# Performance work log

Hardware: AMD Instinct MI355X
Metric: run time of the kernel (lower is better)

The kernel has to match this reference:

```python
import jax, jax.numpy as jnp
import numpy as np

B, Z, U, L, T, D_IN = 64, 512, 2048, 3, 32, 90  # batch, latent, lstm_units, layers, seq_len, output_depth


def setup_inputs() -> dict:
    key = jax.random.key(0)
    ks = jax.random.split(key, 2 + 3 * L + 2)
    s = 0.02
    inp = {"z": jax.random.normal(ks[0], (B, Z), dtype=jnp.float32)}
    inp["w_init"] = jax.random.normal(ks[1], (Z, U * L * 2), dtype=jnp.float32) * s
    inp["b_init"] = jnp.zeros((U * L * 2,), dtype=jnp.float32)
    for i in range(L):
        din = (D_IN + Z) if i == 0 else U
        inp[f"k{i}"] = jax.random.normal(ks[2 + 3 * i], (din, 4 * U), dtype=jnp.float32) * s
        inp[f"rk{i}"] = jax.random.normal(ks[3 + 3 * i], (U, 4 * U), dtype=jnp.float32) * s
        inp[f"b{i}"] = jnp.zeros((4 * U,), dtype=jnp.float32)
    inp["w_out"] = jax.random.normal(ks[-2], (U, D_IN), dtype=jnp.float32) * s
    inp["b_out"] = jnp.zeros((D_IN,), dtype=jnp.float32)
    return inp


def lstm_cell(x, h, c, k, rk, b):
    # Keras LSTMCell: gates in (i, f, g, o) order
    zg = x @ k + h @ rk + b
    i, f, g, o = jnp.split(zg, 4, axis=-1)
    c = jax.nn.sigmoid(f) * c + jax.nn.sigmoid(i) * jnp.tanh(g)
    h = jax.nn.sigmoid(o) * jnp.tanh(c)
    return h, c


def reference(z, w_init, b_init, k0, rk0, b0, k1, rk1, b1, k2, rk2, b2, w_out, b_out):
    Bsz = z.shape[0]
    # z -> initial (h, c) per layer: reshape [B, L, 2, U] -> [L, 2, B, U]
    st = (z @ w_init + b_init).reshape(Bsz, L, 2, U).transpose(1, 2, 0, 3)
    carry = tuple((st[i, 0], st[i, 1]) for i in range(L))
    # generation feeds dummy zero step_input concat z, constant across time
    x = jnp.concatenate([jnp.zeros((Bsz, D_IN), z.dtype), z], axis=-1)
    params = ((k0, rk0, b0), (k1, rk1, b1), (k2, rk2, b2))

    def step(carry, _):
        cin = x
        new = []
        for (k, rk, b), (h, c) in zip(params, carry):
            h, c = lstm_cell(cin, h, c, k, rk, b)
            new.append((h, c))
            cin = h
        logits = cin @ w_out + b_out  # [B, D_IN]
        return tuple(new), logits

    _, ys = jax.lax.scan(step, carry, None, length=T)  # [T, B, D_IN]
    return ys.transpose(1, 0, 2)  # [B, T, D_IN]
```

## Files before the change

### kernel.cpp

```cpp
#include <hip/hip_runtime.h>
#include <cstdint>

#define B_   64
#define Z_   512
#define U_   2048
#define T_   32
#define DIN_ 90
#define G4_  8192
#define STLD 12288

using bf16x8 = __attribute__((ext_vector_type(8))) short;
using f32x4  = __attribute__((ext_vector_type(4))) float;

#define MFMA(a, b, c) __builtin_amdgcn_mfma_f32_16x16x32_bf16((a), (b), (c), 0, 0, 0)

__device__ __forceinline__ unsigned short f2bf(float f) {
    unsigned int u = __float_as_uint(f);
    unsigned int r = (u + 0x7FFFu + ((u >> 16) & 1u)) >> 16;
    return (unsigned short)r;
}
__device__ __forceinline__ float sigf(float x) { return 1.f / (1.f + expf(-x)); }

__device__ __forceinline__ void gld16(const void* g, void* l) {
    __builtin_amdgcn_global_load_lds(
        (const __attribute__((address_space(1))) unsigned int*)g,
        (__attribute__((address_space(3))) unsigned int*)l, 16, 0, 0);
}

#define GEMM_PROLOG()                                                        \
    size_t ag0, ag1, wg0; unsigned al0, al1, wl0;                            \
    {                                                                        \
        int kb0 = (l & 15) << 4;                                             \
        int r0 = wv * 4 + (l >> 4);                        \
        int sw0 = kb0 ^ ((r0 & 7) << 4);                                     \
        ag0 = (size_t)r0 * U_ + (sw0 >> 1);                                  \
        al0 = wv * 1024;                                                     \
        int r1 = 32 + r0;                                 \
        int sw1 = kb0 ^ ((r1 & 7) << 4);                                     \
        ag1 = (size_t)r1 * U_ + (sw1 >> 1);                                  \
        al1 = 8192 + wv * 1024;                                              \
        int rw = r0;                                       \
        int sww = kb0 ^ ((rw & 7) << 4);                                     \
        wg0 = (size_t)(prow0 + rw) * U_ + (sww >> 1);                        \
        wl0 = 16384 + wv * 1024;                                             \
    }                                                                        \
    int aoff[4], woff[4];                                                    \
    {                                                                        \
        const int lkb = (l >> 4) << 4;                                       \
        _Pragma("unroll")                                                    \
        for (int ks = 0; ks < 4; ++ks) {                                     \
            int kb = ks * 64 + lkb;                                          \
            int ar = rq * 16 + lr, wr = ch * 16 + lr;                        \
            aoff[ks] = ar * 256 + (kb ^ ((ar & 7) << 4));                    \
            woff[ks] = 16384 + wr * 256 + (kb ^ ((wr & 7) << 4));            \
        }                                                                    \
    }

#define ISSUE(Ap, Wp, tt) do {                                               \
        const int k0_ = (tt) * 128;                                          \
        char* sb_ = stg + ((tt) % 3) * 24576;                                \
        gld16((Ap) + ag0 + k0_, sb_ + al0);                                  \
        gld16((Ap) + ag1 + k0_, sb_ + al1);                                  \
        gld16((Wp) + wg0 + k0_, sb_ + wl0);                                  \
    } while (0)

#define GEMM_LOOP(Ap, Wp)                                                    \
    ISSUE(Ap, Wp, 0);                                                        \
    ISSUE(Ap, Wp, 1);                                                        \
    for (int tt = 0; tt < 16; ++tt) {                                        \
        if (tt < 15) asm volatile("s_waitcnt vmcnt(3)" ::: "memory");        \
        else         asm volatile("s_waitcnt vmcnt(0)" ::: "memory");        \
        __builtin_amdgcn_s_barrier();                                        \
        if (tt + 2 < 16) ISSUE(Ap, Wp, tt + 2);                              \
        const char* sb = stg + (tt % 3) * 24576;                             \
        _Pragma("unroll")                                                    \
        for (int ks = 0; ks < 4; ++ks) {                                     \
            bf16x8 av = *(const bf16x8*)(sb + aoff[ks]);                     \
            bf16x8 wf = *(const bf16x8*)(sb + woff[ks]);                     \
            acc = MFMA(av, wf, acc);                                         \
        }                                                                    \
    }

#define EPI_ZG(ZG) do {                                                      \
        const int l4_ = (l >> 4) << 2;                                       \
        _Pragma("unroll")                                                    \
        for (int r = 0; r < 4; ++r) {                                        \
            int row = rq * 16 + l4_ + r;                                     \
            int col = prow0 + ch * 16 + lr;                                  \
            __builtin_nontemporal_store(acc[r], &(ZG)[(size_t)row * G4_ + col]); \
        }                                                                    \
    } while (0)

#define EPI_FILL_PLAIN() do {                                                \
        __syncthreads();                         \
        const int l4_ = (l >> 4) << 2;                                       \
        _Pragma("unroll")                                                    \
        for (int r = 0; r < 4; ++r)                                          \
            sg[rq * 16 + l4_ + r][ch * 16 + lr] = acc[r];                    \
    } while (0)

#define EPI_FILL_ZG(ZGIN) do {                                               \
        __syncthreads();                         \
        const int l4_ = (l >> 4) << 2;                                       \
        _Pragma("unroll")                                                    \
        for (int r = 0; r < 4; ++r) {                                        \
            int row = rq * 16 + l4_ + r;                                     \
            int col = prow0 + ch * 16 + lr;                                  \
            sg[row][ch * 16 + lr] =                                          \
                acc[r] + __builtin_nontemporal_load(&(ZGIN)[(size_t)row * G4_ + col]); \
        }                                                                    \
    } while (0)

#define EPI_GATE(BASEEXPR, CST, HNEW) do {                                   \
        __syncthreads();                                                     \
        const int b = t >> 3, uu = t & 7;                                    \
        const int u = blockIdx.x * 8 + uu;                                   \
        float g[4];                                                          \
        _Pragma("unroll")                                                    \
        for (int gi = 0; gi < 4; ++gi)                                       \
            g[gi] = sg[b][gi * 8 + uu] + (BASEEXPR);                         \
        float* cp = (CST) + (size_t)b * U_ + u;                              \
        const float c_ = *cp;                                                \
        const float cn = sigf(g[1]) * c_ + sigf(g[0]) * tanhf(g[2]);         \
        const float hn = sigf(g[3]) * tanhf(cn);                             \
        *cp = cn;                                                            \
        (HNEW)[(size_t)b * U_ + u] = f2bf(hn);                               \
    } while (0)

#define STEP_COMMON()                                                        \
    __shared__ char stg[3 * 24576];                                          \
    auto sg = reinterpret_cast<float(*)[33]>(stg + 2 * 24576);               \
    const int t = threadIdx.x, wv = t >> 6, l = t & 63;                      \
    const int prow0 = blockIdx.x * 32;                                       \
    const int rq = wv & 3, ch = wv >> 2, lr = l & 15;


__global__ __launch_bounds__(256) void transpose_cvt(const float* __restrict__ W,
                                                     unsigned short* __restrict__ Wt,
                                                     int K, int N, int row_off)
{
    __shared__ float tile[32][33];
    const int nb = blockIdx.x * 32, kb = blockIdx.y * 32;
    const int tx = threadIdx.x & 31, ty = threadIdx.x >> 5;
    #pragma unroll
    for (int i = 0; i < 4; ++i)
        tile[ty + i * 8][tx] = W[(size_t)(row_off + kb + ty + i * 8) * N + nb + tx];
    __syncthreads();
    #pragma unroll
    for (int i = 0; i < 4; ++i)
        Wt[(size_t)(nb + ty + i * 8) * K + kb + tx] = f2bf(tile[tx][ty + i * 8]);
}

__global__ __launch_bounds__(256) void transpose_cvt_packed(const float* __restrict__ W,
                                                            unsigned short* __restrict__ Wt)
{
    __shared__ float tile[32][33];
    const int nb = blockIdx.x * 32, kb = blockIdx.y * 32;
    const int tx = threadIdx.x & 31, ty = threadIdx.x >> 5;
    #pragma unroll
    for (int i = 0; i < 4; ++i)
        tile[ty + i * 8][tx] = W[(size_t)(kb + ty + i * 8) * G4_ + nb + tx];
    __syncthreads();
    #pragma unroll
    for (int i = 0; i < 4; ++i) {
        int n = nb + ty + i * 8;
        int g = n >> 11, u = n & 2047;
        int prow = ((u >> 3) << 5) + (g << 3) + (u & 7);
        Wt[(size_t)prow * U_ + kb + tx] = f2bf(tile[tx][ty + i * 8]);
    }
}

__global__ __launch_bounds__(256) void wout_cvt(const float* __restrict__ w_out,
                                                unsigned short* __restrict__ w_outT)
{
    int i = blockIdx.x * 256 + threadIdx.x;
    int d = i >> 11, k = i & 2047;
    w_outT[i] = (d < DIN_) ? f2bf(w_out[(size_t)k * DIN_ + d]) : (unsigned short)0;
}

__global__ __launch_bounds__(256) void cvt_z(const float* __restrict__ z,
                                             unsigned short* __restrict__ zb)
{
    int i = blockIdx.x * 256 + threadIdx.x;
    zb[i] = f2bf(z[i]);
}

__global__ __launch_bounds__(256) void hcinit(const float* __restrict__ st,
                                              unsigned short* __restrict__ h0,
                                              unsigned short* __restrict__ h1,
                                              unsigned short* __restrict__ h2s0,
                                              float* __restrict__ c0,
                                              float* __restrict__ c1,
                                              float* __restrict__ c2)
{
    int idx = blockIdx.x * 256 + threadIdx.x;
    int u = idx & 2047, b = (idx >> 11) & 63, ly = idx >> 17;
    float hv = st[(size_t)b * STLD + ly * 4096 + u];
    float cv = st[(size_t)b * STLD + ly * 4096 + 2048 + u];
    unsigned short* h = (ly == 0) ? h0 : (ly == 1) ? h1 : h2s0;
    float* c = (ly == 0) ? c0 : (ly == 1) ? c1 : c2;
    h[(size_t)b * 2048 + u] = f2bf(hv);
    c[(size_t)b * 2048 + u] = cv;
}

__global__ __launch_bounds__(256) void gemm_plain(const unsigned short* __restrict__ A, int K,
                                                  const unsigned short* __restrict__ Wt,
                                                  const float* __restrict__ bias,
                                                  float* __restrict__ out, int ldo)
{
    const int t = threadIdx.x, wv = t >> 6, l = t & 63;
    const int wm = (wv >> 1) * 32, n0 = blockIdx.x * 64 + (wv & 1) * 32;
    const int lr = l & 15, lk = (l >> 4) * 8;
    f32x4 acc[2][2] = {};
    for (int kt = 0; kt < K; kt += 32) {
        bf16x8 a0 = *(const bf16x8*)(A + (size_t)(wm + lr) * K + kt + lk);
        bf16x8 a1 = *(const bf16x8*)(A + (size_t)(wm + 16 + lr) * K + kt + lk);
        bf16x8 w0 = *(const bf16x8*)(Wt + (size_t)(n0 + lr) * K + kt + lk);
        bf16x8 w1 = *(const bf16x8*)(Wt + (size_t)(n0 + 16 + lr) * K + kt + lk);
        acc[0][0] = MFMA(a0, w0, acc[0][0]);
        acc[0][1] = MFMA(a0, w1, acc[0][1]);
        acc[1][0] = MFMA(a1, w0, acc[1][0]);
        acc[1][1] = MFMA(a1, w1, acc[1][1]);
    }
    #pragma unroll
    for (int mi = 0; mi < 2; ++mi)
        #pragma unroll
        for (int ni = 0; ni < 2; ++ni)
            #pragma unroll
            for (int r = 0; r < 4; ++r) {
                int row = wm + mi * 16 + (l >> 4) * 4 + r;
                int col = n0 + ni * 16 + lr;
                out[(size_t)row * ldo + col] = acc[mi][ni][r] + bias[col];
            }
}

__global__ __launch_bounds__(512) void stepX0(
    const unsigned short* __restrict__ h0old, const unsigned short* __restrict__ rk0P,
    const float* __restrict__ xk0, float* __restrict__ cst0,
    unsigned short* __restrict__ h0new,
    const unsigned short* __restrict__ h1old, const unsigned short* __restrict__ rk1P,
    float* __restrict__ zg1)
{
    STEP_COMMON();
    const int z = blockIdx.y;
    const unsigned short* A = (z == 0) ? h0old : h1old;
    const unsigned short* W = (z == 0) ? rk0P : rk1P;

    GEMM_PROLOG();
    f32x4 acc = {};
    GEMM_LOOP(A, W);

    if (z == 0) {
        EPI_FILL_PLAIN();
        EPI_GATE(xk0[(size_t)b * G4_ + gi * 2048 + u], cst0, h0new);
    } else {
        EPI_ZG(zg1);
    }
}

__global__ __launch_bounds__(512) void stepX(
    const unsigned short* __restrict__ h1prev, const unsigned short* __restrict__ k2P,
    const float* __restrict__ zg2in, const float* __restrict__ b2v,
    float* __restrict__ cst2, unsigned short* __restrict__ h2out,
    const unsigned short* __restrict__ h0old, const unsigned short* __restrict__ rk0P,
    const float* __restrict__ xk0, float* __restrict__ cst0,
    unsigned short* __restrict__ h0new,
    const unsigned short* __restrict__ h1old, const unsigned short* __restrict__ rk1P,
    float* __restrict__ zg1out)
{
    STEP_COMMON();
    const int z = blockIdx.y;
    const unsigned short* A = (z == 0) ? h1prev : (z == 1) ? h0old : h1old;
    const unsigned short* W = (z == 0) ? k2P : (z == 1) ? rk0P : rk1P;

    GEMM_PROLOG();
    f32x4 acc = {};
    GEMM_LOOP(A, W);

    if (z == 0) {
        EPI_FILL_ZG(zg2in);
        EPI_GATE(b2v[gi * 2048 + u], cst2, h2out);
    } else if (z == 1) {
        EPI_FILL_PLAIN();
        EPI_GATE(xk0[(size_t)b * G4_ + gi * 2048 + u], cst0, h0new);
    } else {
        EPI_ZG(zg1out);
    }
}

__global__ __launch_bounds__(512) void stepY(
    const unsigned short* __restrict__ h2cur, const unsigned short* __restrict__ rk2P,
    float* __restrict__ zg2out,
    const unsigned short* __restrict__ h0new, const unsigned short* __restrict__ k1P,
    const float* __restrict__ zg1in, const float* __restrict__ b1v,
    float* __restrict__ cst1, unsigned short* __restrict__ h1new)
{
    STEP_COMMON();
    const int z = blockIdx.y;
    const unsigned short* A = (z == 0) ? h2cur : h0new;
    const unsigned short* W = (z == 0) ? rk2P : k1P;

    GEMM_PROLOG();
    f32x4 acc = {};
    GEMM_LOOP(A, W);

    if (z == 0) {
        EPI_ZG(zg2out);
    } else {
        EPI_FILL_ZG(zg1in);
        EPI_GATE(b1v[gi * 2048 + u], cst1, h1new);
    }
}

__global__ __launch_bounds__(512) void kgate(
    const unsigned short* __restrict__ xNew, const unsigned short* __restrict__ kP,
    const float* __restrict__ zgin, const float* __restrict__ bias,
    float* __restrict__ cst, unsigned short* __restrict__ hNew)
{
    STEP_COMMON();
    GEMM_PROLOG();
    f32x4 acc = {};
    GEMM_LOOP(xNew, kP);

    EPI_FILL_ZG(zgin);
    EPI_GATE(bias[gi * 2048 + u], cst, hNew);
}

__global__ __launch_bounds__(256) void outproj_all(const unsigned short* __restrict__ h2h,
                                                   const unsigned short* __restrict__ w_outT,
                                                   const float* __restrict__ b_out,
                                                   float* __restrict__ out)
{
    const int t = threadIdx.x, wv = t >> 6, l = t & 63;
    const int m0 = blockIdx.x * 64 + wv * 16;
    const int lr = l & 15, lk = (l >> 4) * 8;
    const unsigned short* ap = h2h + (size_t)(m0 + lr) * U_ + lk;
    f32x4 acc[6] = {};
    for (int kt = 0; kt < U_; kt += 32) {
        bf16x8 af = *(const bf16x8*)(ap + kt);
        #pragma unroll
        for (int n = 0; n < 6; ++n) {
            bf16x8 wf = *(const bf16x8*)(w_outT + (size_t)(n * 16 + lr) * U_ + kt + lk);
            acc[n] = MFMA(af, wf, acc[n]);
        }
    }
    const int l4 = (l >> 4) * 4;
    #pragma unroll
    for (int n = 0; n < 6; ++n) {
        const int col = n * 16 + lr;
        if (col < DIN_) {
            #pragma unroll
            for (int r = 0; r < 4; ++r) {
                int row = m0 + l4 + r;
                int tt = row >> 6, b = row & 63;
                out[((size_t)b * T_ + tt) * DIN_ + col] = acc[n][r] + b_out[col];
            }
        }
    }
}

extern "C" void kernel_launch(void* const* d_in, const int* in_sizes, int n_in,
                              void* d_out, int out_size, void* d_ws, size_t ws_size,
                              hipStream_t stream)
{
    const float* z      = (const float*)d_in[0];
    const float* w_init = (const float*)d_in[1];
    const float* b_init = (const float*)d_in[2];
    const float* k0     = (const float*)d_in[3];
    const float* rk0    = (const float*)d_in[4];
    const float* b0     = (const float*)d_in[5];
    const float* k1     = (const float*)d_in[6];
    const float* rk1    = (const float*)d_in[7];
    const float* b1     = (const float*)d_in[8];
    const float* k2     = (const float*)d_in[9];
    const float* rk2    = (const float*)d_in[10];
    const float* b2     = (const float*)d_in[11];
    const float* w_out  = (const float*)d_in[12];
    const float* b_out  = (const float*)d_in[13];
    float* out = (float*)d_out;
    (void)in_sizes; (void)n_in; (void)out_size; (void)ws_size;

    size_t off = 0;
    char* base = (char*)d_ws;
    auto alloc = [&](size_t bytes) { void* p = base + off; off += (bytes + 255) & ~(size_t)255; return p; };
    unsigned short* rk0P = (unsigned short*)alloc((size_t)U_ * G4_ * 2);
    unsigned short* rk1P = (unsigned short*)alloc((size_t)U_ * G4_ * 2);
    unsigned short* rk2P = (unsigned short*)alloc((size_t)U_ * G4_ * 2);
    unsigned short* k1P  = (unsigned short*)alloc((size_t)U_ * G4_ * 2);
    unsigned short* k2P  = (unsigned short*)alloc((size_t)U_ * G4_ * 2);
    unsigned short* wiT  = (unsigned short*)alloc((size_t)STLD * Z_ * 2);
    unsigned short* k0T  = (unsigned short*)alloc((size_t)G4_ * Z_ * 2);
    unsigned short* woT  = (unsigned short*)alloc((size_t)96 * U_ * 2);
    unsigned short* zb   = (unsigned short*)alloc((size_t)B_ * Z_ * 2);
    unsigned short* hb0[2], *hb1[2];
    for (int p = 0; p < 2; ++p) hb0[p] = (unsigned short*)alloc((size_t)B_ * U_ * 2);
    for (int p = 0; p < 2; ++p) hb1[p] = (unsigned short*)alloc((size_t)B_ * U_ * 2);
    unsigned short* h2hist = (unsigned short*)alloc((size_t)(T_ + 1) * B_ * U_ * 2);
    float* st   = (float*)alloc((size_t)B_ * STLD * 4);
    float* xk0  = (float*)alloc((size_t)B_ * G4_ * 4);
    float* zg1  = (float*)alloc((size_t)B_ * G4_ * 4);
    float* zg2  = (float*)alloc((size_t)B_ * G4_ * 4);
    float* cst0 = (float*)alloc((size_t)B_ * U_ * 4);
    float* cst1 = (float*)alloc((size_t)B_ * U_ * 4);
    float* cst2 = (float*)alloc((size_t)B_ * U_ * 4);

    transpose_cvt_packed<<<dim3(G4_ / 32, U_ / 32), 256, 0, stream>>>(rk0, rk0P);
    transpose_cvt_packed<<<dim3(G4_ / 32, U_ / 32), 256, 0, stream>>>(rk1, rk1P);
    transpose_cvt_packed<<<dim3(G4_ / 32, U_ / 32), 256, 0, stream>>>(rk2, rk2P);
    transpose_cvt_packed<<<dim3(G4_ / 32, U_ / 32), 256, 0, stream>>>(k1, k1P);
    transpose_cvt_packed<<<dim3(G4_ / 32, U_ / 32), 256, 0, stream>>>(k2, k2P);
    transpose_cvt<<<dim3(STLD / 32, Z_ / 32), 256, 0, stream>>>(w_init, wiT, Z_, STLD, 0);
    transpose_cvt<<<dim3(G4_ / 32, Z_ / 32), 256, 0, stream>>>(k0, k0T, Z_, G4_, DIN_);
    wout_cvt<<<dim3(96 * U_ / 256), 256, 0, stream>>>(w_out, woT);
    cvt_z<<<dim3(B_ * Z_ / 256), 256, 0, stream>>>(z, zb);

    gemm_plain<<<dim3(STLD / 64), 256, 0, stream>>>(zb, Z_, wiT, b_init, st, STLD);
    gemm_plain<<<dim3(G4_ / 64), 256, 0, stream>>>(zb, Z_, k0T, b0, xk0, G4_);
    hcinit<<<dim3(3 * B_ * U_ / 256), 256, 0, stream>>>(st, hb0[0], hb1[0], h2hist,
                                                        cst0, cst1, cst2);

    stepX0<<<dim3(U_ / 8, 2), 512, 0, stream>>>(hb0[0], rk0P, xk0, cst0, hb0[1],
                                                hb1[0], rk1P, zg1);
    stepY<<<dim3(U_ / 8, 2), 512, 0, stream>>>(h2hist, rk2P, zg2,
                                               hb0[1], k1P, zg1, b1, cst1, hb1[1]);
    for (int tstep = 1; tstep < T_; ++tstep) {
        const int p = tstep & 1;
        stepX<<<dim3(U_ / 8, 3), 512, 0, stream>>>(
            hb1[p], k2P, zg2, b2, cst2, h2hist + (size_t)tstep * B_ * U_,
            hb0[p], rk0P, xk0, cst0, hb0[p ^ 1],
            hb1[p], rk1P, zg1);
        stepY<<<dim3(U_ / 8, 2), 512, 0, stream>>>(
            h2hist + (size_t)tstep * B_ * U_, rk2P, zg2,
            hb0[p ^ 1], k1P, zg1, b1, cst1, hb1[p ^ 1]);
    }
    kgate<<<dim3(U_ / 8), 512, 0, stream>>>(hb1[0], k2P, zg2, b2, cst2,
                                            h2hist + (size_t)T_ * B_ * U_);
    outproj_all<<<dim3(T_ * B_ / 64), 256, 0, stream>>>(h2hist + (size_t)B_ * U_, woT, b_out, out);
}
```

Before: 1.487 ms.

## Fuse recurrent LSTM steps into a persistent cooperative kernel with grid syncs

Replaces the per-timestep stepX/stepY kernel launches with a single cooperative kernel of 256 blocks. Each block serially processes the X-phase and Y-phase tile jobs, with grid-wide barriers between phases. The goal is to remove launch overhead and inter-kernel gaps. The trade-off is less concurrent work per phase, since each block now runs several jobs in sequence, plus grid sync costs. A fallback multi-launch path is kept for when the cooperative launch fails.

```diff
diff --git a/kernel.cpp b/kernel.cpp
--- a/kernel.cpp
+++ b/kernel.cpp
@@ -1,5 +1,8 @@
 #include <hip/hip_runtime.h>
+#include <hip/hip_cooperative_groups.h>
 #include <cstdint>
+
+namespace cg = cooperative_groups;
 
 #define B_   64
 #define Z_   512
@@ -31,7 +34,7 @@
     size_t ag0, ag1, wg0; unsigned al0, al1, wl0;                            \
     {                                                                        \
         int kb0 = (l & 15) << 4;                                             \
-        int r0 = wv * 4 + (l >> 4);                        \
+        int r0 = wv * 4 + (l >> 4);                          \
         int sw0 = kb0 ^ ((r0 & 7) << 4);                                     \
         ag0 = (size_t)r0 * U_ + (sw0 >> 1);                                  \
         al0 = wv * 1024;                                                     \
@@ -39,9 +42,7 @@
         int sw1 = kb0 ^ ((r1 & 7) << 4);                                     \
         ag1 = (size_t)r1 * U_ + (sw1 >> 1);                                  \
         al1 = 8192 + wv * 1024;                                              \
-        int rw = r0;                                       \
-        int sww = kb0 ^ ((rw & 7) << 4);                                     \
-        wg0 = (size_t)(prow0 + rw) * U_ + (sww >> 1);                        \
+        wg0 = (size_t)r0 * U_ + (sw0 >> 1);                \
         wl0 = 16384 + wv * 1024;                                             \
     }                                                                        \
     int aoff[4], woff[4];                                                    \
@@ -86,7 +87,7 @@
         _Pragma("unroll")                                                    \
         for (int r = 0; r < 4; ++r) {                                        \
             int row = rq * 16 + l4_ + r;                                     \
-            int col = prow0 + ch * 16 + lr;                                  \
+            int col = til * 32 + ch * 16 + lr;                               \
             __builtin_nontemporal_store(acc[r], &(ZG)[(size_t)row * G4_ + col]); \
         }                                                                    \
     } while (0)
@@ -105,7 +106,7 @@
         _Pragma("unroll")                                                    \
         for (int r = 0; r < 4; ++r) {                                        \
             int row = rq * 16 + l4_ + r;                                     \
-            int col = prow0 + ch * 16 + lr;                                  \
+            int col = til * 32 + ch * 16 + lr;                               \
             sg[row][ch * 16 + lr] =                                          \
                 acc[r] + __builtin_nontemporal_load(&(ZGIN)[(size_t)row * G4_ + col]); \
         }                                                                    \
@@ -114,7 +115,7 @@
 #define EPI_GATE(BASEEXPR, CST, HNEW) do {                                   \
         __syncthreads();                                                     \
         const int b = t >> 3, uu = t & 7;                                    \
-        const int u = blockIdx.x * 8 + uu;                                   \
+        const int u = til * 8 + uu;                                          \
         float g[4];                                                          \
         _Pragma("unroll")                                                    \
         for (int gi = 0; gi < 4; ++gi)                                       \
@@ -127,12 +128,63 @@
         (HNEW)[(size_t)b * U_ + u] = f2bf(hn);                               \
     } while (0)
 
-#define STEP_COMMON()                                                        \
+#define XJOB(JOB, TSTEP, P) do {                                             \
+        if ((JOB) < 256) {                                                   \
+            if ((TSTEP) >= 1) {                                              \
+                const int til = (JOB);                                       \
+                const unsigned short* Aj = h1b[(P)];                         \
+                const unsigned short* Wj = k2P + (size_t)til * 32 * U_;      \
+                f32x4 acc = {};                                              \
+                GEMM_LOOP(Aj, Wj);                                           \
+                EPI_FILL_ZG(zg2);                                            \
+                EPI_GATE(b2v[gi * 2048 + u], cst2,                           \
+                         h2hist + (size_t)(TSTEP) * B_ * U_);                \
+            }                                                                \
+        } else if ((JOB) < 512) {                                            \
+            const int til = (JOB) - 256;                                     \
+            const unsigned short* Aj = h0b[(P)];                             \
+            const unsigned short* Wj = rk0P + (size_t)til * 32 * U_;         \
+            f32x4 acc = {};                                                  \
+            GEMM_LOOP(Aj, Wj);                                               \
+            EPI_FILL_PLAIN();                                                \
+            EPI_GATE(xk0[(size_t)b * G4_ + gi * 2048 + u], cst0,             \
+                     h0b[(P) ^ 1]);                                          \
+        } else {                                                             \
+            const int til = (JOB) - 512;                                     \
+            const unsigned short* Aj = h1b[(P)];                             \
+            const unsigned short* Wj = rk1P + (size_t)til * 32 * U_;         \
+            f32x4 acc = {};                                                  \
+            GEMM_LOOP(Aj, Wj);                                               \
+            EPI_ZG(zg1);                                                     \
+        }                                                                    \
+    } while (0)
+
+#define YJOB(JOB, TSTEP, P) do {                                             \
+        if ((JOB) < 256) {                                                   \
+            const int til = (JOB);                                           \
+            const unsigned short* Aj = h2hist + (size_t)(TSTEP) * B_ * U_;   \
+            const unsigned short* Wj = rk2P + (size_t)til * 32 * U_;         \
+            f32x4 acc = {};                                                  \
+            GEMM_LOOP(Aj, Wj);                                               \
+            EPI_ZG(zg2);                                                     \
+        } else {                                                             \
+            const int til = (JOB) - 256;                                     \
+            const unsigned short* Aj = h0b[(P) ^ 1];                         \
+            const unsigned short* Wj = k1P + (size_t)til * 32 * U_;          \
+            f32x4 acc = {};                                                  \
+            GEMM_LOOP(Aj, Wj);                                               \
+            EPI_FILL_ZG(zg1);                                                \
+            EPI_GATE(b1v[gi * 2048 + u], cst1, h1b[(P) ^ 1]);                \
+        }                                                                    \
+    } while (0)
+
+#define STEP_LOCALS()                                                        \
     __shared__ char stg[3 * 24576];                                          \
     auto sg = reinterpret_cast<float(*)[33]>(stg + 2 * 24576);               \
     const int t = threadIdx.x, wv = t >> 6, l = t & 63;                      \
-    const int prow0 = blockIdx.x * 32;                                       \
-    const int rq = wv & 3, ch = wv >> 2, lr = l & 15;
+    const int rq = wv & 3, ch = wv >> 2, lr = l & 15;                        \
+    unsigned short* h0b[2] = {h0b0, h0b1};                                   \
+    unsigned short* h1b[2] = {h1b0, h1b1};
 
 
 __global__ __launch_bounds__(256) void transpose_cvt(const float* __restrict__ W,
@@ -234,96 +286,71 @@
             }
 }
 
-__global__ __launch_bounds__(512) void stepX0(
-    const unsigned short* __restrict__ h0old, const unsigned short* __restrict__ rk0P,
-    const float* __restrict__ xk0, float* __restrict__ cst0,
-    unsigned short* __restrict__ h0new,
-    const unsigned short* __restrict__ h1old, const unsigned short* __restrict__ rk1P,
-    float* __restrict__ zg1)
-{
-    STEP_COMMON();
-    const int z = blockIdx.y;
-    const unsigned short* A = (z == 0) ? h0old : h1old;
-    const unsigned short* W = (z == 0) ? rk0P : rk1P;
-
+__global__ __launch_bounds__(512, 2) void lstm_loop(
+    unsigned short* h0b0, unsigned short* h0b1,
+    unsigned short* h1b0, unsigned short* h1b1,
+    unsigned short* h2hist,
+    const unsigned short* rk0P, const unsigned short* rk1P, const unsigned short* rk2P,
+    const unsigned short* k1P, const unsigned short* k2P,
+    const float* xk0, const float* b1v, const float* b2v,
+    float* zg1, float* zg2,
+    float* cst0, float* cst1, float* cst2)
+{
+    STEP_LOCALS();
+    cg::grid_group grid = cg::this_grid();
+    const int blk = blockIdx.x;
     GEMM_PROLOG();
-    f32x4 acc = {};
-    GEMM_LOOP(A, W);
-
-    if (z == 0) {
-        EPI_FILL_PLAIN();
-        EPI_GATE(xk0[(size_t)b * G4_ + gi * 2048 + u], cst0, h0new);
-    } else {
-        EPI_ZG(zg1);
-    }
-}
-
-__global__ __launch_bounds__(512) void stepX(
-    const unsigned short* __restrict__ h1prev, const unsigned short* __restrict__ k2P,
-    const float* __restrict__ zg2in, const float* __restrict__ b2v,
-    float* __restrict__ cst2, unsigned short* __restrict__ h2out,
-    const unsigned short* __restrict__ h0old, const unsigned short* __restrict__ rk0P,
-    const float* __restrict__ xk0, float* __restrict__ cst0,
-    unsigned short* __restrict__ h0new,
-    const unsigned short* __restrict__ h1old, const unsigned short* __restrict__ rk1P,
-    float* __restrict__ zg1out)
-{
-    STEP_COMMON();
-    const int z = blockIdx.y;
-    const unsigned short* A = (z == 0) ? h1prev : (z == 1) ? h0old : h1old;
-    const unsigned short* W = (z == 0) ? k2P : (z == 1) ? rk0P : rk1P;
-
+
+    for (int tstep = 0; tstep <= T_; ++tstep) {
+        const int p = tstep & 1;
+        XJOB(blk, tstep, p);
+        if (tstep == T_) break;
+        __syncthreads();
+        XJOB(blk + 256, tstep, p);
+        __syncthreads();
+        XJOB(blk + 512, tstep, p);
+        grid.sync();
+        YJOB(blk, tstep, p);
+        __syncthreads();
+        YJOB(blk + 256, tstep, p);
+        grid.sync();
+    }
+}
+
+__global__ __launch_bounds__(512, 2) void fbX(
+    unsigned short* h0b0, unsigned short* h0b1,
+    unsigned short* h1b0, unsigned short* h1b1,
+    unsigned short* h2hist,
+    const unsigned short* rk0P, const unsigned short* rk1P, const unsigned short* rk2P,
+    const unsigned short* k1P, const unsigned short* k2P,
+    const float* xk0, const float* b1v, const float* b2v,
+    float* zg1, float* zg2,
+    float* cst0, float* cst1, float* cst2, int tstep)
+{
+    STEP_LOCALS();
+    (void)rk2P; (void)k1P; (void)b1v; (void)cst1;
     GEMM_PROLOG();
-    f32x4 acc = {};
-    GEMM_LOOP(A, W);
-
-    if (z == 0) {
-        EPI_FILL_ZG(zg2in);
-        EPI_GATE(b2v[gi * 2048 + u], cst2, h2out);
-    } else if (z == 1) {
-        EPI_FILL_PLAIN();
-        EPI_GATE(xk0[(size_t)b * G4_ + gi * 2048 + u], cst0, h0new);
-    } else {
-        EPI_ZG(zg1out);
-    }
-}
-
-__global__ __launch_bounds__(512) void stepY(
-    const unsigned short* __restrict__ h2cur, const unsigned short* __restrict__ rk2P,
-    float* __restrict__ zg2out,
-    const unsigned short* __restrict__ h0new, const unsigned short* __restrict__ k1P,
-    const float* __restrict__ zg1in, const float* __restrict__ b1v,
-    float* __restrict__ cst1, unsigned short* __restrict__ h1new)
-{
-    STEP_COMMON();
-    const int z = blockIdx.y;
-    const unsigned short* A = (z == 0) ? h2cur : h0new;
-    const unsigned short* W = (z == 0) ? rk2P : k1P;
-
+    const int p = tstep & 1;
+    const int job = blockIdx.y * 256 + blockIdx.x;
+    XJOB(job, tstep, p);
+}
+
+__global__ __launch_bounds__(512, 2) void fbY(
+    unsigned short* h0b0, unsigned short* h0b1,
+    unsigned short* h1b0, unsigned short* h1b1,
+    unsigned short* h2hist,
+    const unsigned short* rk0P, const unsigned short* rk1P, const unsigned short* rk2P,
+    const unsigned short* k1P, const unsigned short* k2P,
+    const float* xk0, const float* b1v, const float* b2v,
+    float* zg1, float* zg2,
+    float* cst0, float* cst1, float* cst2, int tstep)
+{
+    STEP_LOCALS();
+    (void)rk0P; (void)k2P; (void)b2v; (void)cst0; (void)cst2; (void)xk0;
     GEMM_PROLOG();
-    f32x4 acc = {};
-    GEMM_LOOP(A, W);
-
-    if (z == 0) {
-        EPI_ZG(zg2out);
-    } else {
-        EPI_FILL_ZG(zg1in);
-        EPI_GATE(b1v[gi * 2048 + u], cst1, h1new);
-    }
-}
-
-__global__ __launch_bounds__(512) void kgate(
-    const unsigned short* __restrict__ xNew, const unsigned short* __restrict__ kP,
-    const float* __restrict__ zgin, const float* __restrict__ bias,
-    float* __restrict__ cst, unsigned short* __restrict__ hNew)
-{
-    STEP_COMMON();
-    GEMM_PROLOG();
-    f32x4 acc = {};
-    GEMM_LOOP(xNew, kP);
-
-    EPI_FILL_ZG(zgin);
-    EPI_GATE(bias[gi * 2048 + u], cst, hNew);
+    const int p = tstep & 1;
+    const int job = blockIdx.y * 256 + blockIdx.x;
+    YJOB(job, tstep, p);
 }
 
 __global__ __launch_bounds__(256) void outproj_all(const unsigned short* __restrict__ h2h,
@@ -419,21 +446,29 @@
     hcinit<<<dim3(3 * B_ * U_ / 256), 256, 0, stream>>>(st, hb0[0], hb1[0], h2hist,
                                                         cst0, cst1, cst2);
 
-    stepX0<<<dim3(U_ / 8, 2), 512, 0, stream>>>(hb0[0], rk0P, xk0, cst0, hb0[1],
-                                                hb1[0], rk1P, zg1);
-    stepY<<<dim3(U_ / 8, 2), 512, 0, stream>>>(h2hist, rk2P, zg2,
-                                               hb0[1], k1P, zg1, b1, cst1, hb1[1]);
-    for (int tstep = 1; tstep < T_; ++tstep) {
-        const int p = tstep & 1;
-        stepX<<<dim3(U_ / 8, 3), 512, 0, stream>>>(
-            hb1[p], k2P, zg2, b2, cst2, h2hist + (size_t)tstep * B_ * U_,
-            hb0[p], rk0P, xk0, cst0, hb0[p ^ 1],
-            hb1[p], rk1P, zg1);
-        stepY<<<dim3(U_ / 8, 2), 512, 0, stream>>>(
-            h2hist + (size_t)tstep * B_ * U_, rk2P, zg2,
-            hb0[p ^ 1], k1P, zg1, b1, cst1, hb1[p ^ 1]);
-    }
-    kgate<<<dim3(U_ / 8), 512, 0, stream>>>(hb1[0], k2P, zg2, b2, cst2,
-                                            h2hist + (size_t)T_ * B_ * U_);
+    void* kargs[] = {
+        &hb0[0], &hb0[1], &hb1[0], &hb1[1], &h2hist,
+        &rk0P, &rk1P, &rk2P, &k1P, &k2P,
+        (void*)&xk0, (void*)&b1, (void*)&b2,
+        &zg1, &zg2, &cst0, &cst1, &cst2,
+    };
+    hipError_t cerr = hipLaunchCooperativeKernel((const void*)lstm_loop, dim3(256),
+                                                 dim3(512), kargs, 0, stream);
+    if (cerr != hipSuccess) {
+        for (int tstep = 0; tstep < T_; ++tstep) {
+            fbX<<<dim3(256, 3), 512, 0, stream>>>(hb0[0], hb0[1], hb1[0], hb1[1], h2hist,
+                                                  rk0P, rk1P, rk2P, k1P, k2P,
+                                                  xk0, b1, b2, zg1, zg2,
+                                                  cst0, cst1, cst2, tstep);
+            fbY<<<dim3(256, 2), 512, 0, stream>>>(hb0[0], hb0[1], hb1[0], hb1[1], h2hist,
+                                                  rk0P, rk1P, rk2P, k1P, k2P,
+                                                  xk0, b1, b2, zg1, zg2,
+                                                  cst0, cst1, cst2, tstep);
+        }
+        fbX<<<dim3(256, 1), 512, 0, stream>>>(hb0[0], hb0[1], hb1[0], hb1[1], h2hist,
+                                              rk0P, rk1P, rk2P, k1P, k2P,
+                                              xk0, b1, b2, zg1, zg2,
+                                              cst0, cst1, cst2, T_);
+    }
     outproj_all<<<dim3(T_ * B_ / 64), 256, 0, stream>>>(h2hist + (size_t)B_ * U_, woT, b_out, out);
 }
```

After: 4.105 ms. +176.1%, slower.
